# Kernel optimization log

Measured on AMD Instinct MI355X. Metric: run time of the kernel, lower is better.

Reference implementation:

```python
import jax, jax.numpy as jnp
import numpy as np

B, STREAM, IN_CH = 128, 512, 4
EXTRA, GROUPS, DEPTH = 5, 2, 3
STEP, LENGTH = 16, 32
RNN, OUT = 256, 10
C = IN_CH + 1 + EXTRA              # augmented channels: original + time + 1x1-conv
SIG_C = C + C * C + C ** 3          # signature channels per group at depth 3
W = (STREAM - LENGTH) // STEP + 1   # number of sliding windows = GRU steps
F = GROUPS * SIG_C                  # GRU input features


def _outer(a, b):
    # flattened tensor (outer) product on last axis: (...,m),(...,n)->(...,m*n)
    return (a[..., :, None] * b[..., None, :]).reshape(a.shape[:-1] + (a.shape[-1] * b.shape[-1],))


def _chen_step(S, dx):
    # Chen's identity: S <- S (tensor) exp(dx). S is a tuple of flattened
    # signature levels (..., C^k), k=1..DEPTH; dx has shape (..., C).
    P = [jnp.ones(dx.shape[:-1] + (1,), dx.dtype)]  # dx^{(x)j}/j!, j=0..DEPTH
    for j in range(1, DEPTH + 1):
        P.append(_outer(P[-1], dx) / j)
    newS = []
    for k in range(1, DEPTH + 1):
        acc = P[k]  # S_0 (x) P_k
        for j in range(k):
            acc = acc + _outer(S[k - 1 - j], P[j])
        newS.append(acc)
    return tuple(newS)


def setup_inputs() -> dict:
    key = jax.random.key(0)
    ks = jax.random.split(key, 10)
    s_aug = 1.0 / np.sqrt(IN_CH)
    s_rnn = 1.0 / np.sqrt(RNN)
    return {
        "x": jax.random.normal(ks[0], (B, STREAM, IN_CH), jnp.float32),
        "W_aug": jax.random.uniform(ks[1], (GROUPS, EXTRA, IN_CH), jnp.float32, -s_aug, s_aug),
        "b_aug": jax.random.uniform(ks[2], (GROUPS, EXTRA), jnp.float32, -s_aug, s_aug),
        "W_ih": jax.random.uniform(ks[3], (3 * RNN, F), jnp.float32, -s_rnn, s_rnn),
        "W_hh": jax.random.uniform(ks[4], (3 * RNN, RNN), jnp.float32, -s_rnn, s_rnn),
        "b_ih": jax.random.uniform(ks[5], (3 * RNN,), jnp.float32, -s_rnn, s_rnn),
        "b_hh": jax.random.uniform(ks[6], (3 * RNN,), jnp.float32, -s_rnn, s_rnn),
        "W_out": jax.random.uniform(ks[7], (OUT, RNN), jnp.float32, -s_rnn, s_rnn),
        "b_out": jax.random.uniform(ks[8], (OUT,), jnp.float32, -s_rnn, s_rnn),
    }


def reference(x, W_aug, b_aug, W_ih, W_hh, b_ih, b_hh, W_out, b_out):
    # (a) linear augmentation per channel group: [original | time | conv1x1(x)]
    t = jnp.linspace(0.0, 1.0, STREAM, dtype=x.dtype)
    t = jnp.broadcast_to(t[None, :, None], (B, STREAM, 1))
    aug = jnp.einsum('bsi,gei->bgse', x, W_aug) + b_aug[None, :, None, :]  # (B,G,S,EXTRA)
    base = jnp.broadcast_to(jnp.concatenate([x, t], -1)[:, None],
                            (B, GROUPS, STREAM, IN_CH + 1))
    xa = jnp.concatenate([base, aug], -1)            # (B,G,S,C)
    xa = xa.reshape(B * GROUPS, STREAM, C)

    # (b) depth-3 signatures over sliding windows via Chen's identity
    dx = xa[:, 1:] - xa[:, :-1]                       # (BG, S-1, C)
    widx = jnp.arange(W)[:, None] * STEP + jnp.arange(LENGTH - 1)[None, :]
    dxw = dx[:, widx]                                 # (BG, W, L-1, C)
    dxw = jnp.moveaxis(dxw, 2, 0)                     # (L-1, BG, W, C)
    S0 = tuple(jnp.zeros((B * GROUPS, W, C ** k), x.dtype) for k in range(1, DEPTH + 1))
    S, _ = jax.lax.scan(lambda S, d: (_chen_step(S, d), None), S0, dxw)
    sig = jnp.concatenate(S, -1)                      # (BG, W, SIG_C)
    sig = sig.reshape(B, GROUPS, W, SIG_C)
    sig = jnp.moveaxis(sig, 2, 0).reshape(W, B, F)    # (W, B, G*SIG_C)

    # (c) GRU over window signatures (torch.nn.GRUCell math, gate order r,z,n)
    def gru(h, xt):
        gi = xt @ W_ih.T + b_ih
        gh = h @ W_hh.T + b_hh
        ir, iz, inn = jnp.split(gi, 3, -1)
        hr, hz, hn = jnp.split(gh, 3, -1)
        r = jax.nn.sigmoid(ir + hr)
        z = jax.nn.sigmoid(iz + hz)
        n = jnp.tanh(inn + r * hn)
        return (1 - z) * n + z * h, None

    h, _ = jax.lax.scan(gru, jnp.zeros((B, RNN), x.dtype), sig)
    return jax.nn.sigmoid(h @ W_out.T + b_out)        # (B, OUT)
```

## Files before the change

kernel.cpp:

```cpp
#include <hip/hip_runtime.h>
#include <hip/hip_bf16.h>
#include <stdint.h>


typedef _Float16 f16;
typedef f16  f16x2 __attribute__((ext_vector_type(2)));
typedef f16  f16x4 __attribute__((ext_vector_type(4)));
typedef f16  f16x8 __attribute__((ext_vector_type(8)));
typedef float f32x2 __attribute__((ext_vector_type(2)));
typedef float f32x4 __attribute__((ext_vector_type(4)));

#define ASYNC16(gp, lp) __builtin_amdgcn_global_load_lds( \
    (const __attribute__((address_space(1))) void*)(gp),  \
    (__attribute__((address_space(3))) void*)(lp), 16, 0, 0)

#define BAR_LDS() do { asm volatile("s_waitcnt lgkmcnt(0)" ::: "memory"); \
                       __builtin_amdgcn_s_barrier();                      \
                       asm volatile("" ::: "memory"); } while (0)

__device__ __forceinline__ float fexp2(float x) {
    float r; asm("v_exp_f32 %0, %1" : "=v"(r) : "v"(x)); return r;
}
__device__ __forceinline__ float frcp(float x) {
    float r; asm("v_rcp_f32 %0, %1" : "=v"(r) : "v"(x)); return r;
}

__global__ __launch_bounds__(256) void prep_kernel(const float* __restrict__ x,
                                                   const float* __restrict__ W_aug,
                                                   const float* __restrict__ Wih,
                                                   const float* __restrict__ Whh,
                                                   f16* __restrict__ sig16,
                                                   f16* __restrict__ wih16,
                                                   f16* __restrict__ whh16,
                                                   uint8_t* __restrict__ whh8) {
    __shared__ float dxs[4][31][10];
    const int tid = threadIdx.x;
    if (blockIdx.x < 840) {
        int c = blockIdx.x * 256 + tid;
        int r = c / 280, kc = (c - r * 280) * 8;
        const float* src = Wih + (size_t)r * 2220 + kc;
        f16x8 o;
        if (kc + 8 <= 2220) {
            float4 v0 = *(const float4*)(src);
            float4 v1 = *(const float4*)(src + 4);
            o[0]=(f16)v0.x; o[1]=(f16)v0.y; o[2]=(f16)v0.z; o[3]=(f16)v0.w;
            o[4]=(f16)v1.x; o[5]=(f16)v1.y; o[6]=(f16)v1.z; o[7]=(f16)v1.w;
        } else {
#pragma unroll
            for (int j = 0; j < 8; j++)
                o[j] = (f16)((kc + j < 2220) ? src[j] : 0.0f);
        }
        *(f16x8*)(wih16 + (size_t)r * 2240 + kc) = o;
        return;
    }
    if (blockIdx.x < 936) {
        int c2 = ((int)blockIdx.x - 840) * 256 + tid;
        int j8 = c2 * 8;
        float w[8];
        {
            float4 v0 = *(const float4*)(Whh + j8);
            float4 v1 = *(const float4*)(Whh + j8 + 4);
            w[0]=v0.x; w[1]=v0.y; w[2]=v0.z; w[3]=v0.w;
            w[4]=v1.x; w[5]=v1.y; w[6]=v1.z; w[7]=v1.w;
        }
        f16x8 o;
#pragma unroll
        for (int j = 0; j < 8; j++) o[j] = (f16)w[j];
        *(f16x8*)(whh16 + j8) = o;
        if (j8 < 131072) {
            uint32_t p01 = (uint32_t)__builtin_amdgcn_cvt_pk_fp8_f32(w[0]*16.f, w[1]*16.f, 0, false) & 0xffffu;
            uint32_t p23 = (uint32_t)__builtin_amdgcn_cvt_pk_fp8_f32(w[2]*16.f, w[3]*16.f, 0, false) & 0xffffu;
            uint32_t p45 = (uint32_t)__builtin_amdgcn_cvt_pk_fp8_f32(w[4]*16.f, w[5]*16.f, 0, false) & 0xffffu;
            uint32_t p67 = (uint32_t)__builtin_amdgcn_cvt_pk_fp8_f32(w[6]*16.f, w[7]*16.f, 0, false) & 0xffffu;
            uint2 st = make_uint2(p01 | (p23 << 16), p45 | (p67 << 16));
            *(uint2*)(whh8 + j8) = st;
        }
        return;
    }
    const int sub = tid >> 6, t64 = tid & 63;
    const int cid = ((int)blockIdx.x - 936) * 4 + sub;
    const int w = cid % 31;
    const int bg = cid / 31;
    const int b = bg >> 1, g = bg & 1;
    if (t64 < 31) {
        int s = w * 16 + t64;
        const float4 x0 = *(const float4*)(x + ((size_t)b * 512 + s) * 4);
        const float4 x1 = *(const float4*)(x + ((size_t)b * 512 + s + 1) * 4);
        float d0 = x1.x - x0.x, d1 = x1.y - x0.y, d2 = x1.z - x0.z, d3 = x1.w - x0.w;
        dxs[sub][t64][0] = d0; dxs[sub][t64][1] = d1;
        dxs[sub][t64][2] = d2; dxs[sub][t64][3] = d3;
        dxs[sub][t64][4] = 1.0f / 511.0f;
#pragma unroll
        for (int e = 0; e < 5; e++) {
            const float* wa = W_aug + (g * 5 + e) * 4;
            dxs[sub][t64][5 + e] = d0 * wa[0] + d1 * wa[1] + d2 * wa[2] + d3 * wa[3];
        }
    }
    __syncthreads();
    size_t base = ((size_t)(w * 128 + b)) * 2240 + (size_t)g * 1110;
    if (t64 < 50) {
        int p0 = 2 * t64, p1 = p0 + 1;
        int i0 = p0 / 10, j0 = p0 % 10, j1 = j0 + 1;
        const float* dz  = &dxs[sub][0][0];
        const float* pI  = dz + i0;
        const float* pJ0 = dz + j0;
        const float* pJ1 = dz + j1;
        float s3a[10], s3b[10];
#pragma unroll
        for (int k = 0; k < 10; k++) { s3a[k] = 0.f; s3b[k] = 0.f; }
        float s2a = 0.f, s2b = 0.f, s1 = 0.f;
        for (int l = 0; l < 31; l++) {
            const float* row = dz + l * 10;
            float di  = pI[l * 10];
            float dj0 = pJ0[l * 10];
            float dj1 = pJ1[l * 10];
            float t0 = s1 + di * (1.0f / 3.0f);
            float a0 = s2a + t0 * (0.5f * dj0);
            float a1 = s2b + t0 * (0.5f * dj1);
#pragma unroll
            for (int k = 0; k < 10; k++) {
                float dk = row[k];
                s3a[k] += a0 * dk;
                s3b[k] += a1 * dk;
            }
            float u = s1 + 0.5f * di;
            s2a += u * dj0;
            s2b += u * dj1;
            s1 += di;
        }
        *(f16x2*)(sig16 + base + 10 + p0) = (f16x2){(f16)s2a, (f16)s2b};
#pragma unroll
        for (int k = 0; k < 5; k++)
            *(f16x2*)(sig16 + base + 110 + p0 * 10 + 2 * k) =
                (f16x2){(f16)s3a[2 * k], (f16)s3a[2 * k + 1]};
#pragma unroll
        for (int k = 0; k < 5; k++)
            *(f16x2*)(sig16 + base + 110 + p1 * 10 + 2 * k) =
                (f16x2){(f16)s3b[2 * k], (f16)s3b[2 * k + 1]};
    } else if (t64 < 60) {
        int c = t64 - 50;
        const float* pc = &dxs[sub][0][0] + c;
        float s = 0.f;
        for (int l = 0; l < 31; l++) s += pc[l * 10];
        sig16[base + c] = (f16)s;
    }
    if (g == 1 && t64 < 10)
        *(f16x2*)(sig16 + ((size_t)(w * 128 + b)) * 2240 + 2220 + 2 * t64) =
            (f16x2){(f16)0.0f, (f16)0.0f};
}

__global__ __launch_bounds__(512) void gemm_kernel(const f16* __restrict__ A,
                                                   const f16* __restrict__ Bw,
                                                   const float* __restrict__ bias,
                                                   const float* __restrict__ bhh,
                                                   f16* __restrict__ Cgi) {
    const int lin = blockIdx.x;
    const int t = (lin & 7) + 8 * (lin / 48);
    const int nb = (lin >> 3) % 6;
    if (t >= 31) return;
    __shared__ __align__(16) f16 As[7][128 * 32];
    __shared__ __align__(16) f16 Bs[7][128 * 32];
    const int tid = threadIdx.x, lane = tid & 63, wid = tid >> 6;
    const int wm = wid >> 2, wn = wid & 3;
    const int Mbase = t * 128, Nbase = nb * 128;
    const int lr = lane >> 2, lk = lane & 3;
    const int l16 = lane & 15, quad = lane >> 4;
    const int r0 = wid * 16;
    const f16* gaA0 = A  + (size_t)(Mbase + r0 + lr) * 2240 + lk * 8;
    const f16* gbB0 = Bw + (size_t)(Nbase + r0 + lr) * 2240 + lk * 8;

#define GISSUE(KT, BUF) do { \
        int _k0 = (KT) * 32; \
        ASYNC16(gaA0 + _k0, &As[BUF][r0 * 32]); \
        ASYNC16(gbB0 + _k0, &Bs[BUF][r0 * 32]); } while (0)

#define GCOMPUTE(BUF) do { \
        f16x8 af[4], bf[2]; \
        _Pragma("unroll") \
        for (int mt = 0; mt < 4; mt++) \
            af[mt] = *(const f16x8*)&As[BUF][(wm * 64 + mt * 16 + l16) * 32 + quad * 8]; \
        _Pragma("unroll") \
        for (int nt = 0; nt < 2; nt++) \
            bf[nt] = *(const f16x8*)&Bs[BUF][(wn * 32 + nt * 16 + l16) * 32 + quad * 8]; \
        _Pragma("unroll") \
        for (int mt = 0; mt < 4; mt++) \
            _Pragma("unroll") \
            for (int nt = 0; nt < 2; nt++) \
                acc[mt][nt] = __builtin_amdgcn_mfma_f32_16x16x32_f16(af[mt], bf[nt], acc[mt][nt], 0, 0, 0); } while (0)

    f32x4 acc[4][2];
#pragma unroll
    for (int mt = 0; mt < 4; mt++)
#pragma unroll
        for (int nt = 0; nt < 2; nt++) acc[mt][nt] = (f32x4){0.f, 0.f, 0.f, 0.f};

    GISSUE(0, 0); GISSUE(1, 1); GISSUE(2, 2);
    GISSUE(3, 3); GISSUE(4, 4); GISSUE(5, 5);
    for (int kt = 0; kt < 64; kt++) {
        asm volatile("s_waitcnt vmcnt(10) lgkmcnt(0)\n\ts_barrier" ::: "memory");
        GISSUE(kt + 6, (kt + 6) % 7);
        GCOMPUTE(kt % 7);
    }
    asm volatile("s_waitcnt vmcnt(0) lgkmcnt(0)\n\ts_barrier" ::: "memory");
    GCOMPUTE(1); GCOMPUTE(2); GCOMPUTE(3);
    GCOMPUTE(4); GCOMPUTE(5); GCOMPUTE(6);

    const float NEG_LOG2E = -1.4426950408889634f;
    const float TWO_LOG2E =  2.8853900817779268f;
#pragma unroll
    for (int mt = 0; mt < 4; mt++) {
        const int bbv = wm * 4 + mt;
#pragma unroll
        for (int nt = 0; nt < 2; nt++) {
            int col = Nbase + wn * 32 + nt * 16 + l16;
            float bvv = bias[col] + (col < 512 ? bhh[col] : 0.0f);
            float scl = (col < 512) ? NEG_LOG2E : TWO_LOG2E;
            int gs = col >> 8, hcc = col & 255;
            int gw = hcc >> 5, gtc = (hcc >> 4) & 1, gl = hcc & 15;
            int u = gs * 2 + gtc;
            int gtid = gw * 64 + quad * 16 + gl;
            size_t off = ((size_t)((t * 8 + bbv) * 6 + u)) * 2048 + (size_t)gtid * 4;
            f16x4 st;
#pragma unroll
            for (int rr = 0; rr < 4; rr++) st[rr] = (f16)((acc[mt][nt][rr] + bvv) * scl);
            *(f16x4*)(Cgi + off) = st;
        }
    }
#undef GISSUE
#undef GCOMPUTE
}

#define ACLOB \
  "a0","a1","a2","a3","a4","a5","a6","a7","a8","a9","a10","a11","a12","a13","a14","a15", \
  "a16","a17","a18","a19","a20","a21","a22","a23","a24","a25","a26","a27","a28","a29","a30","a31", \
  "a32","a33","a34","a35","a36","a37","a38","a39","a40","a41","a42","a43","a44","a45","a46","a47", \
  "a48","a49","a50","a51","a52","a53","a54","a55","a56","a57","a58","a59","a60","a61","a62","a63", \
  "a64","a65","a66","a67","a68","a69","a70","a71","a72","a73","a74","a75","a76","a77","a78","a79", \
  "a80","a81","a82","a83","a84","a85","a86","a87","a88","a89","a90","a91","a92","a93","a94","a95", \
  "a96","a97","a98","a99","a100","a101","a102","a103","a104","a105","a106","a107","a108","a109","a110","a111", \
  "a112","a113","a114","a115","a116","a117","a118","a119","a120","a121","a122","a123","a124","a125","a126","a127"

#define LF8(A0,A1, U, KT) do { \
  f32x2 _t = *(const f32x2*)(whh8 + (size_t)(((U) >> 1) * 256 + wid * 32 + ((U) & 1) * 16 + l16) * 256 + (KT) * 32 + quad * 8); \
  asm volatile("v_accvgpr_write_b32 a" #A0 ", %0\n\t" \
               "v_accvgpr_write_b32 a" #A1 ", %1" \
               :: "v"(_t[0]), "v"(_t[1]) : "a" #A0, "a" #A1); } while (0)

#define LFN(A0,A1,A2,A3, TC, KT) do { \
  f32x4 _t = *(const f32x4*)(whh16 + (size_t)(512 + wid * 32 + (TC) * 16 + l16) * 256 + (KT) * 32 + quad * 8); \
  asm volatile("v_accvgpr_write_b32 a" #A0 ", %0\n\t" \
               "v_accvgpr_write_b32 a" #A1 ", %1\n\t" \
               "v_accvgpr_write_b32 a" #A2 ", %2\n\t" \
               "v_accvgpr_write_b32 a" #A3 ", %3" \
               :: "v"(_t[0]), "v"(_t[1]), "v"(_t[2]), "v"(_t[3]) \
               : "a" #A0, "a" #A1, "a" #A2, "a" #A3); } while (0)

#define FP8GZ(P, F0,F1,F2,F3) \
  "v_mfma_f32_16x16x32_fp8_fp8 %[aR0], " P ", a[" F0 "], %[zq]\n\t" \
  "v_mfma_f32_16x16x32_fp8_fp8 %[aR1], " P ", a[" F1 "], %[zq]\n\t" \
  "v_mfma_f32_16x16x32_fp8_fp8 %[aZ0], " P ", a[" F2 "], %[zq]\n\t" \
  "v_mfma_f32_16x16x32_fp8_fp8 %[aZ1], " P ", a[" F3 "], %[zq]\n\t"

#define FP8G(P, F0,F1,F2,F3) \
  "v_mfma_f32_16x16x32_fp8_fp8 %[aR0], " P ", a[" F0 "], %[aR0]\n\t" \
  "v_mfma_f32_16x16x32_fp8_fp8 %[aR1], " P ", a[" F1 "], %[aR1]\n\t" \
  "v_mfma_f32_16x16x32_fp8_fp8 %[aZ0], " P ", a[" F2 "], %[aZ0]\n\t" \
  "v_mfma_f32_16x16x32_fp8_fp8 %[aZ1], " P ", a[" F3 "], %[aZ1]\n\t"

#define F16GZ(Q, G0,G1) \
  "v_mfma_f32_16x16x32_f16 %[aN0], " Q ", a[" G0 "], %[zq]\n\t" \
  "v_mfma_f32_16x16x32_f16 %[aN1], " Q ", a[" G1 "], %[zq]\n\t"

#define F16G(Q, G0,G1) \
  "v_mfma_f32_16x16x32_f16 %[aN0], " Q ", a[" G0 "], %[aN0]\n\t" \
  "v_mfma_f32_16x16x32_f16 %[aN1], " Q ", a[" G1 "], %[aN1]\n\t"

__global__ __launch_bounds__(512, 2) void gru_kernel(const f16* __restrict__ gi,
                                                     const f16* __restrict__ whh16,
                                                     const uint8_t* __restrict__ whh8,
                                                     const float* __restrict__ b_hh,
                                                     const float* __restrict__ W_out,
                                                     const float* __restrict__ b_out,
                                                     float* __restrict__ out) {
    __shared__ __align__(16) f16 hbufF[2][16 * 280];
    __shared__ __align__(16) uint8_t hbuf8[2][16 * 272];
    const int tid = threadIdx.x, lane = tid & 63, wid = tid >> 6;
    const int quad = lane >> 4, l16 = lane & 15;
    const int bb = blockIdx.x;

    for (int i = tid; i < 16 * 280; i += 512) hbufF[1][i] = (f16)0.0f;
    for (int i = tid; i < 16 * 272; i += 512) hbuf8[1][i] = 0;

    LF8(0,1, 0,0);   LF8(2,3, 0,1);   LF8(4,5, 0,2);   LF8(6,7, 0,3);
    LF8(8,9, 0,4);   LF8(10,11, 0,5); LF8(12,13, 0,6); LF8(14,15, 0,7);
    LF8(16,17, 1,0); LF8(18,19, 1,1); LF8(20,21, 1,2); LF8(22,23, 1,3);
    LF8(24,25, 1,4); LF8(26,27, 1,5); LF8(28,29, 1,6); LF8(30,31, 1,7);
    LF8(32,33, 2,0); LF8(34,35, 2,1); LF8(36,37, 2,2); LF8(38,39, 2,3);
    LF8(40,41, 2,4); LF8(42,43, 2,5); LF8(44,45, 2,6); LF8(46,47, 2,7);
    LF8(48,49, 3,0); LF8(50,51, 3,1); LF8(52,53, 3,2); LF8(54,55, 3,3);
    LF8(56,57, 3,4); LF8(58,59, 3,5); LF8(60,61, 3,6); LF8(62,63, 3,7);
    LFN(64,65,66,67,   0,0); LFN(68,69,70,71,   0,1); LFN(72,73,74,75,   0,2); LFN(76,77,78,79,   0,3);
    LFN(80,81,82,83,   0,4); LFN(84,85,86,87,   0,5); LFN(88,89,90,91,   0,6); LFN(92,93,94,95,   0,7);
    LFN(96,97,98,99,   1,0); LFN(100,101,102,103, 1,1); LFN(104,105,106,107, 1,2); LFN(108,109,110,111, 1,3);
    LFN(112,113,114,115, 1,4); LFN(116,117,118,119, 1,5); LFN(120,121,122,123, 1,6); LFN(124,125,126,127, 1,7);

    const float C2 = 2.8853900817779268f;
    float bhn[2];
#pragma unroll
    for (int tc = 0; tc < 2; tc++) bhn[tc] = C2 * b_hh[512 + wid * 32 + tc * 16 + l16];
    float hm[2][4];
#pragma unroll
    for (int tc = 0; tc < 2; tc++)
#pragma unroll
        for (int rr = 0; rr < 4; rr++) hm[tc][rr] = 0.f;

    uint32_t aF0 = (uint32_t)(uintptr_t)(__attribute__((address_space(3))) const void*)
                       (&hbufF[0][l16 * 280 + quad * 8]);
    uint32_t aF1 = (uint32_t)(uintptr_t)(__attribute__((address_space(3))) const void*)
                       (&hbufF[1][l16 * 280 + quad * 8]);
    uint32_t a80 = (uint32_t)(uintptr_t)(__attribute__((address_space(3))) const void*)
                       (&hbuf8[0][l16 * 272 + quad * 8]);
    uint32_t a81 = (uint32_t)(uintptr_t)(__attribute__((address_space(3))) const void*)
                       (&hbuf8[1][l16 * 272 + quad * 8]);

    const size_t lanebase = (size_t)bb * 12288 + (size_t)tid * 4;
    f16x4 gcur[6];
#pragma unroll
    for (int u = 0; u < 6; u++)
        gcur[u] = *(const f16x4*)(gi + lanebase + u * 2048);

    const f32x4 zq = (f32x4){0.f, 0.f, 0.f, 0.f};

    BAR_LDS();

    for (int t = 0; t < 31; t++) {
        const uint32_t a8 = (t & 1) ? a80 : a81;
        const uint32_t aF = (t & 1) ? aF0 : aF1;
        f32x4 aR0, aR1, aZ0, aZ1, aN0, aN1;
        f32x2 p0, p1, p2;
        f32x4 q0, q1, q2;
        asm volatile(
            "s_setprio 1\n\t"
            "ds_read_b64  %[p0], %[a8] offset:0\n\t"
            "ds_read_b128 %[q0], %[aF] offset:0\n\t"
            "ds_read_b64  %[p1], %[a8] offset:32\n\t"
            "ds_read_b128 %[q1], %[aF] offset:64\n\t"
            "ds_read_b64  %[p2], %[a8] offset:64\n\t"
            "ds_read_b128 %[q2], %[aF] offset:128\n\t"
            "s_waitcnt lgkmcnt(5)\n\t"
            FP8GZ("%[p0]", "0:1","16:17","32:33","48:49")
            "ds_read_b64  %[p0], %[a8] offset:96\n\t"
            "s_waitcnt lgkmcnt(5)\n\t"
            F16GZ("%[q0]", "64:67","96:99")
            "ds_read_b128 %[q0], %[aF] offset:192\n\t"
            "s_waitcnt lgkmcnt(5)\n\t"
            FP8G("%[p1]", "2:3","18:19","34:35","50:51")
            "ds_read_b64  %[p1], %[a8] offset:128\n\t"
            "s_waitcnt lgkmcnt(5)\n\t"
            F16G("%[q1]", "68:71","100:103")
            "ds_read_b128 %[q1], %[aF] offset:256\n\t"
            "s_waitcnt lgkmcnt(5)\n\t"
            FP8G("%[p2]", "4:5","20:21","36:37","52:53")
            "ds_read_b64  %[p2], %[a8] offset:160\n\t"
            "s_waitcnt lgkmcnt(5)\n\t"
            F16G("%[q2]", "72:75","104:107")
            "ds_read_b128 %[q2], %[aF] offset:320\n\t"
            "s_waitcnt lgkmcnt(5)\n\t"
            FP8G("%[p0]", "6:7","22:23","38:39","54:55")
            "ds_read_b64  %[p0], %[a8] offset:192\n\t"
            "s_waitcnt lgkmcnt(5)\n\t"
            F16G("%[q0]", "76:79","108:111")
            "ds_read_b128 %[q0], %[aF] offset:384\n\t"
            "s_waitcnt lgkmcnt(5)\n\t"
            FP8G("%[p1]", "8:9","24:25","40:41","56:57")
            "ds_read_b64  %[p1], %[a8] offset:224\n\t"
            "s_waitcnt lgkmcnt(5)\n\t"
            F16G("%[q1]", "80:83","112:115")
            "ds_read_b128 %[q1], %[aF] offset:448\n\t"
            "s_waitcnt lgkmcnt(5)\n\t"
            FP8G("%[p2]", "10:11","26:27","42:43","58:59")
            "s_waitcnt lgkmcnt(4)\n\t"
            F16G("%[q2]", "84:87","116:119")
            "s_waitcnt lgkmcnt(3)\n\t"
            FP8G("%[p0]", "12:13","28:29","44:45","60:61")
            "s_waitcnt lgkmcnt(2)\n\t"
            F16G("%[q0]", "88:91","120:123")
            "s_waitcnt lgkmcnt(1)\n\t"
            FP8G("%[p1]", "14:15","30:31","46:47","62:63")
            "s_waitcnt lgkmcnt(0)\n\t"
            F16G("%[q1]", "92:95","124:127")
            "s_setprio 0\n\t"
            "s_nop 7\n\ts_nop 7"
            : [aR0]"=&v"(aR0), [aR1]"=&v"(aR1), [aZ0]"=&v"(aZ0), [aZ1]"=&v"(aZ1),
              [aN0]"=&v"(aN0), [aN1]"=&v"(aN1),
              [p0]"=&v"(p0), [p1]"=&v"(p1), [p2]"=&v"(p2),
              [q0]"=&v"(q0), [q1]"=&v"(q1), [q2]"=&v"(q2)
            : [a8]"v"(a8), [aF]"v"(aF), [zq]"v"(zq)
            : ACLOB);

        f16* hdF = hbufF[t & 1];
        uint8_t* hd8 = hbuf8[t & 1];
        const float C1N16 = -0.09016844005556021f;
#pragma unroll
        for (int tc = 0; tc < 2; tc++) {
            const int hcx = wid * 32 + tc * 16 + l16;
            const f32x4 vR = tc ? aR1 : aR0;
            const f32x4 vZ = tc ? aZ1 : aZ0;
            const f32x4 vN = tc ? aN1 : aN0;
#pragma unroll
            for (int rr = 0; rr < 4; rr++) {
                float rg = frcp(1.f + fexp2(fmaf(C1N16, vR[rr], (float)gcur[tc][rr])));
                float zg = frcp(1.f + fexp2(fmaf(C1N16, vZ[rr], (float)gcur[2 + tc][rr])));
                float t2 = fmaf(rg, fmaf(C2, vN[rr], bhn[tc]), (float)gcur[4 + tc][rr]);
                float e2 = fexp2(t2);
                float ng = fmaf(-2.f, frcp(e2 + 1.f), 1.f);
                float h  = fmaf(zg, hm[tc][rr] - ng, ng);
                hm[tc][rr] = h;
                hdF[(quad * 4 + rr) * 280 + hcx] = (f16)h;
                int pk = __builtin_amdgcn_cvt_pk_fp8_f32(h, h, 0, false);
                hd8[(quad * 4 + rr) * 272 + hcx] = (uint8_t)pk;
            }
        }
        {
            int tn = (t < 30) ? t + 1 : 30;
            const f16* gsrc = gi + (size_t)tn * 98304 + lanebase;
#pragma unroll
            for (int u = 0; u < 6; u++)
                gcur[u] = *(const f16x4*)(gsrc + u * 2048);
        }
        BAR_LDS();
    }
    if (tid < 160) {
        int r = tid / 10, oc = tid - r * 10;
        const f16* hfin = hbufF[0];
        float s = b_out[oc];
        for (int k = 0; k < 256; k++) s += (float)hfin[r * 280 + k] * W_out[oc * 256 + k];
        out[(bb * 16 + r) * 10 + oc] = frcp(1.f + __expf(-s));
    }
}

extern "C" void kernel_launch(void* const* d_in, const int* in_sizes, int n_in,
                              void* d_out, int out_size, void* d_ws, size_t ws_size,
                              hipStream_t stream) {
    const float* x     = (const float*)d_in[0];
    const float* W_aug = (const float*)d_in[1];
    const float* W_ih  = (const float*)d_in[3];
    const float* W_hh  = (const float*)d_in[4];
    const float* b_ih  = (const float*)d_in[5];
    const float* b_hh  = (const float*)d_in[6];
    const float* W_out = (const float*)d_in[7];
    const float* b_out = (const float*)d_in[8];
    float* out = (float*)d_out;

    char* ws = (char*)d_ws;
    const size_t SIG_BYTES  = (size_t)3968 * 2240 * 2;
    const size_t WIH_BYTES  = (size_t)768 * 2240 * 2;
    const size_t WHH_BYTES  = (size_t)768 * 256 * 2;
    const size_t WHH8_BYTES = (size_t)512 * 256;
    const size_t GI_BYTES   = (size_t)31 * 8 * 6 * 512 * 4 * 2;
    if (ws_size < SIG_BYTES + WIH_BYTES + WHH_BYTES + WHH8_BYTES + GI_BYTES) return;
    f16* sig16    = (f16*)ws;
    f16* wih16    = (f16*)(ws + SIG_BYTES);
    f16* whh16    = (f16*)(ws + SIG_BYTES + WIH_BYTES);
    uint8_t* whh8 = (uint8_t*)(ws + SIG_BYTES + WIH_BYTES + WHH_BYTES);
    f16* giw      = (f16*)(ws + SIG_BYTES + WIH_BYTES + WHH_BYTES + WHH8_BYTES);

    hipLaunchKernelGGL(prep_kernel, dim3(2920), dim3(256), 0, stream,
                       x, W_aug, W_ih, W_hh, sig16, wih16, whh16, whh8);
    hipLaunchKernelGGL(gemm_kernel, dim3(192), dim3(512), 0, stream,
                       sig16, wih16, b_ih, b_hh, giw);
    hipLaunchKernelGGL(gru_kernel, dim3(8), dim3(512), 0, stream,
                       giw, whh16, whh8, b_hh, W_out, b_out, out);
}
```

Baseline: 200.0 us.

## Fuse input GEMM and GRU kernels with an atomic completion counter

```diff
diff --git a/kernel.cpp b/kernel.cpp
--- a/kernel.cpp
+++ b/kernel.cpp
@@ -32,7 +32,8 @@
                                                    f16* __restrict__ sig16,
                                                    f16* __restrict__ wih16,
                                                    f16* __restrict__ whh16,
-                                                   uint8_t* __restrict__ whh8) {
+                                                   uint8_t* __restrict__ whh8,
+                                                   unsigned int* __restrict__ done) {
     __shared__ float dxs[4][31][10];
     const int tid = threadIdx.x;
     if (blockIdx.x < 840) {
@@ -54,6 +55,7 @@
         return;
     }
     if (blockIdx.x < 936) {
+        if (blockIdx.x == 840 && tid == 0) *done = 0u;
         int c2 = ((int)blockIdx.x - 840) * 256 + tid;
         int j8 = c2 * 8;
         float w[8];
@@ -149,25 +151,80 @@
             (f16x2){(f16)0.0f, (f16)0.0f};
 }
 
-__global__ __launch_bounds__(512) void gemm_kernel(const f16* __restrict__ A,
-                                                   const f16* __restrict__ Bw,
-                                                   const float* __restrict__ bias,
-                                                   const float* __restrict__ bhh,
-                                                   f16* __restrict__ Cgi) {
-    const int lin = blockIdx.x;
-    const int t = (lin & 7) + 8 * (lin / 48);
-    const int nb = (lin >> 3) % 6;
-    if (t >= 31) return;
+#define ACLOB \
+  "a0","a1","a2","a3","a4","a5","a6","a7","a8","a9","a10","a11","a12","a13","a14","a15", \
+  "a16","a17","a18","a19","a20","a21","a22","a23","a24","a25","a26","a27","a28","a29","a30","a31", \
+  "a32","a33","a34","a35","a36","a37","a38","a39","a40","a41","a42","a43","a44","a45","a46","a47", \
+  "a48","a49","a50","a51","a52","a53","a54","a55","a56","a57","a58","a59","a60","a61","a62","a63", \
+  "a64","a65","a66","a67","a68","a69","a70","a71","a72","a73","a74","a75","a76","a77","a78","a79", \
+  "a80","a81","a82","a83","a84","a85","a86","a87","a88","a89","a90","a91","a92","a93","a94","a95", \
+  "a96","a97","a98","a99","a100","a101","a102","a103","a104","a105","a106","a107","a108","a109","a110","a111", \
+  "a112","a113","a114","a115","a116","a117","a118","a119","a120","a121","a122","a123","a124","a125","a126","a127"
+
+#define LF8(A0,A1, U, KT) do { \
+  f32x2 _t = *(const f32x2*)(whh8 + (size_t)(((U) >> 1) * 256 + wid * 32 + ((U) & 1) * 16 + l16) * 256 + (KT) * 32 + quad * 8); \
+  asm volatile("v_accvgpr_write_b32 a" #A0 ", %0\n\t" \
+               "v_accvgpr_write_b32 a" #A1 ", %1" \
+               :: "v"(_t[0]), "v"(_t[1]) : "a" #A0, "a" #A1); } while (0)
+
+#define LFN(A0,A1,A2,A3, TC, KT) do { \
+  f32x4 _t = *(const f32x4*)(whh16 + (size_t)(512 + wid * 32 + (TC) * 16 + l16) * 256 + (KT) * 32 + quad * 8); \
+  asm volatile("v_accvgpr_write_b32 a" #A0 ", %0\n\t" \
+               "v_accvgpr_write_b32 a" #A1 ", %1\n\t" \
+               "v_accvgpr_write_b32 a" #A2 ", %2\n\t" \
+               "v_accvgpr_write_b32 a" #A3 ", %3" \
+               :: "v"(_t[0]), "v"(_t[1]), "v"(_t[2]), "v"(_t[3]) \
+               : "a" #A0, "a" #A1, "a" #A2, "a" #A3); } while (0)
+
+#define FP8GZ(P, F0,F1,F2,F3) \
+  "v_mfma_f32_16x16x32_fp8_fp8 %[aR0], " P ", a[" F0 "], %[zq]\n\t" \
+  "v_mfma_f32_16x16x32_fp8_fp8 %[aR1], " P ", a[" F1 "], %[zq]\n\t" \
+  "v_mfma_f32_16x16x32_fp8_fp8 %[aZ0], " P ", a[" F2 "], %[zq]\n\t" \
+  "v_mfma_f32_16x16x32_fp8_fp8 %[aZ1], " P ", a[" F3 "], %[zq]\n\t"
+
+#define FP8G(P, F0,F1,F2,F3) \
+  "v_mfma_f32_16x16x32_fp8_fp8 %[aR0], " P ", a[" F0 "], %[aR0]\n\t" \
+  "v_mfma_f32_16x16x32_fp8_fp8 %[aR1], " P ", a[" F1 "], %[aR1]\n\t" \
+  "v_mfma_f32_16x16x32_fp8_fp8 %[aZ0], " P ", a[" F2 "], %[aZ0]\n\t" \
+  "v_mfma_f32_16x16x32_fp8_fp8 %[aZ1], " P ", a[" F3 "], %[aZ1]\n\t"
+
+#define F16GZ(Q, G0,G1) \
+  "v_mfma_f32_16x16x32_f16 %[aN0], " Q ", a[" G0 "], %[zq]\n\t" \
+  "v_mfma_f32_16x16x32_f16 %[aN1], " Q ", a[" G1 "], %[zq]\n\t"
+
+#define F16G(Q, G0,G1) \
+  "v_mfma_f32_16x16x32_f16 %[aN0], " Q ", a[" G0 "], %[aN0]\n\t" \
+  "v_mfma_f32_16x16x32_f16 %[aN1], " Q ", a[" G1 "], %[aN1]\n\t"
+
+__global__ __launch_bounds__(512, 2) void fused_kernel(const f16* __restrict__ A,
+                                                       const f16* __restrict__ Bw,
+                                                       const float* __restrict__ bias,
+                                                       const float* __restrict__ bhh,
+                                                       f16* __restrict__ Cgi,
+                                                       const f16* __restrict__ whh16,
+                                                       const uint8_t* __restrict__ whh8,
+                                                       const float* __restrict__ W_out,
+                                                       const float* __restrict__ b_out,
+                                                       float* __restrict__ out,
+                                                       unsigned int* __restrict__ done) {
     __shared__ __align__(16) f16 As[7][128 * 32];
     __shared__ __align__(16) f16 Bs[7][128 * 32];
+    __shared__ __align__(16) f16 hbufF[2][16 * 280];
+    __shared__ __align__(16) uint8_t hbuf8[2][16 * 272];
     const int tid = threadIdx.x, lane = tid & 63, wid = tid >> 6;
-    const int wm = wid >> 2, wn = wid & 3;
-    const int Mbase = t * 128, Nbase = nb * 128;
-    const int lr = lane >> 2, lk = lane & 3;
-    const int l16 = lane & 15, quad = lane >> 4;
-    const int r0 = wid * 16;
-    const f16* gaA0 = A  + (size_t)(Mbase + r0 + lr) * 2240 + lk * 8;
-    const f16* gbB0 = Bw + (size_t)(Nbase + r0 + lr) * 2240 + lk * 8;
+    const int quad = lane >> 4, l16 = lane & 15;
+
+    if (blockIdx.x < 192) {
+        const int lin = blockIdx.x;
+        const int t = (lin & 7) + 8 * (lin / 48);
+        const int nb = (lin >> 3) % 6;
+        if (t >= 31) return;
+        const int wm = wid >> 2, wn = wid & 3;
+        const int Mbase = t * 128, Nbase = nb * 128;
+        const int lr = lane >> 2, lk = lane & 3;
+        const int r0 = wid * 16;
+        const f16* gaA0 = A  + (size_t)(Mbase + r0 + lr) * 2240 + lk * 8;
+        const f16* gbB0 = Bw + (size_t)(Nbase + r0 + lr) * 2240 + lk * 8;
 
 #define GISSUE(KT, BUF) do { \
         int _k0 = (KT) * 32; \
@@ -188,105 +245,54 @@
             for (int nt = 0; nt < 2; nt++) \
                 acc[mt][nt] = __builtin_amdgcn_mfma_f32_16x16x32_f16(af[mt], bf[nt], acc[mt][nt], 0, 0, 0); } while (0)
 
-    f32x4 acc[4][2];
-#pragma unroll
-    for (int mt = 0; mt < 4; mt++)
-#pragma unroll
-        for (int nt = 0; nt < 2; nt++) acc[mt][nt] = (f32x4){0.f, 0.f, 0.f, 0.f};
-
-    GISSUE(0, 0); GISSUE(1, 1); GISSUE(2, 2);
-    GISSUE(3, 3); GISSUE(4, 4); GISSUE(5, 5);
-    for (int kt = 0; kt < 64; kt++) {
-        asm volatile("s_waitcnt vmcnt(10) lgkmcnt(0)\n\ts_barrier" ::: "memory");
-        GISSUE(kt + 6, (kt + 6) % 7);
-        GCOMPUTE(kt % 7);
-    }
-    asm volatile("s_waitcnt vmcnt(0) lgkmcnt(0)\n\ts_barrier" ::: "memory");
-    GCOMPUTE(1); GCOMPUTE(2); GCOMPUTE(3);
-    GCOMPUTE(4); GCOMPUTE(5); GCOMPUTE(6);
-
-    const float NEG_LOG2E = -1.4426950408889634f;
-    const float TWO_LOG2E =  2.8853900817779268f;
-#pragma unroll
-    for (int mt = 0; mt < 4; mt++) {
-        const int bbv = wm * 4 + mt;
-#pragma unroll
-        for (int nt = 0; nt < 2; nt++) {
-            int col = Nbase + wn * 32 + nt * 16 + l16;
-            float bvv = bias[col] + (col < 512 ? bhh[col] : 0.0f);
-            float scl = (col < 512) ? NEG_LOG2E : TWO_LOG2E;
-            int gs = col >> 8, hcc = col & 255;
-            int gw = hcc >> 5, gtc = (hcc >> 4) & 1, gl = hcc & 15;
-            int u = gs * 2 + gtc;
-            int gtid = gw * 64 + quad * 16 + gl;
-            size_t off = ((size_t)((t * 8 + bbv) * 6 + u)) * 2048 + (size_t)gtid * 4;
-            f16x4 st;
-#pragma unroll
-            for (int rr = 0; rr < 4; rr++) st[rr] = (f16)((acc[mt][nt][rr] + bvv) * scl);
-            *(f16x4*)(Cgi + off) = st;
-        }
-    }
+        f32x4 acc[4][2];
+#pragma unroll
+        for (int mt = 0; mt < 4; mt++)
+#pragma unroll
+            for (int nt = 0; nt < 2; nt++) acc[mt][nt] = (f32x4){0.f, 0.f, 0.f, 0.f};
+
+        GISSUE(0, 0); GISSUE(1, 1); GISSUE(2, 2);
+        GISSUE(3, 3); GISSUE(4, 4); GISSUE(5, 5);
+        for (int kt = 0; kt < 64; kt++) {
+            asm volatile("s_waitcnt vmcnt(10) lgkmcnt(0)\n\ts_barrier" ::: "memory");
+            GISSUE(kt + 6, (kt + 6) % 7);
+            GCOMPUTE(kt % 7);
+        }
+        asm volatile("s_waitcnt vmcnt(0) lgkmcnt(0)\n\ts_barrier" ::: "memory");
+        GCOMPUTE(1); GCOMPUTE(2); GCOMPUTE(3);
+        GCOMPUTE(4); GCOMPUTE(5); GCOMPUTE(6);
+
+        const float NEG_LOG2E = -1.4426950408889634f;
+        const float TWO_LOG2E =  2.8853900817779268f;
+#pragma unroll
+        for (int mt = 0; mt < 4; mt++) {
+            const int bbv = wm * 4 + mt;
+#pragma unroll
+            for (int nt = 0; nt < 2; nt++) {
+                int col = Nbase + wn * 32 + nt * 16 + l16;
+                float bvv = bias[col] + (col < 512 ? bhh[col] : 0.0f);
+                float scl = (col < 512) ? NEG_LOG2E : TWO_LOG2E;
+                int gs = col >> 8, hcc = col & 255;
+                int gw = hcc >> 5, gtc = (hcc >> 4) & 1, gl = hcc & 15;
+                int u = gs * 2 + gtc;
+                int gtid = gw * 64 + quad * 16 + gl;
+                size_t off = ((size_t)((t * 8 + bbv) * 6 + u)) * 2048 + (size_t)gtid * 4;
+                f16x4 st;
+#pragma unroll
+                for (int rr = 0; rr < 4; rr++) st[rr] = (f16)((acc[mt][nt][rr] + bvv) * scl);
+                *(f16x4*)(Cgi + off) = st;
+            }
+        }
+        __threadfence();
+        __syncthreads();
+        if (tid == 0) atomicAdd(done, 1u);
+        return;
 #undef GISSUE
 #undef GCOMPUTE
-}
-
-#define ACLOB \
-  "a0","a1","a2","a3","a4","a5","a6","a7","a8","a9","a10","a11","a12","a13","a14","a15", \
-  "a16","a17","a18","a19","a20","a21","a22","a23","a24","a25","a26","a27","a28","a29","a30","a31", \
-  "a32","a33","a34","a35","a36","a37","a38","a39","a40","a41","a42","a43","a44","a45","a46","a47", \
-  "a48","a49","a50","a51","a52","a53","a54","a55","a56","a57","a58","a59","a60","a61","a62","a63", \
-  "a64","a65","a66","a67","a68","a69","a70","a71","a72","a73","a74","a75","a76","a77","a78","a79", \
-  "a80","a81","a82","a83","a84","a85","a86","a87","a88","a89","a90","a91","a92","a93","a94","a95", \
-  "a96","a97","a98","a99","a100","a101","a102","a103","a104","a105","a106","a107","a108","a109","a110","a111", \
-  "a112","a113","a114","a115","a116","a117","a118","a119","a120","a121","a122","a123","a124","a125","a126","a127"
-
-#define LF8(A0,A1, U, KT) do { \
-  f32x2 _t = *(const f32x2*)(whh8 + (size_t)(((U) >> 1) * 256 + wid * 32 + ((U) & 1) * 16 + l16) * 256 + (KT) * 32 + quad * 8); \
-  asm volatile("v_accvgpr_write_b32 a" #A0 ", %0\n\t" \
-               "v_accvgpr_write_b32 a" #A1 ", %1" \
-               :: "v"(_t[0]), "v"(_t[1]) : "a" #A0, "a" #A1); } while (0)
-
-#define LFN(A0,A1,A2,A3, TC, KT) do { \
-  f32x4 _t = *(const f32x4*)(whh16 + (size_t)(512 + wid * 32 + (TC) * 16 + l16) * 256 + (KT) * 32 + quad * 8); \
-  asm volatile("v_accvgpr_write_b32 a" #A0 ", %0\n\t" \
-               "v_accvgpr_write_b32 a" #A1 ", %1\n\t" \
-               "v_accvgpr_write_b32 a" #A2 ", %2\n\t" \
-               "v_accvgpr_write_b32 a" #A3 ", %3" \
-               :: "v"(_t[0]), "v"(_t[1]), "v"(_t[2]), "v"(_t[3]) \
-               : "a" #A0, "a" #A1, "a" #A2, "a" #A3); } while (0)
-
-#define FP8GZ(P, F0,F1,F2,F3) \
-  "v_mfma_f32_16x16x32_fp8_fp8 %[aR0], " P ", a[" F0 "], %[zq]\n\t" \
-  "v_mfma_f32_16x16x32_fp8_fp8 %[aR1], " P ", a[" F1 "], %[zq]\n\t" \
-  "v_mfma_f32_16x16x32_fp8_fp8 %[aZ0], " P ", a[" F2 "], %[zq]\n\t" \
-  "v_mfma_f32_16x16x32_fp8_fp8 %[aZ1], " P ", a[" F3 "], %[zq]\n\t"
-
-#define FP8G(P, F0,F1,F2,F3) \
-  "v_mfma_f32_16x16x32_fp8_fp8 %[aR0], " P ", a[" F0 "], %[aR0]\n\t" \
-  "v_mfma_f32_16x16x32_fp8_fp8 %[aR1], " P ", a[" F1 "], %[aR1]\n\t" \
-  "v_mfma_f32_16x16x32_fp8_fp8 %[aZ0], " P ", a[" F2 "], %[aZ0]\n\t" \
-  "v_mfma_f32_16x16x32_fp8_fp8 %[aZ1], " P ", a[" F3 "], %[aZ1]\n\t"
-
-#define F16GZ(Q, G0,G1) \
-  "v_mfma_f32_16x16x32_f16 %[aN0], " Q ", a[" G0 "], %[zq]\n\t" \
-  "v_mfma_f32_16x16x32_f16 %[aN1], " Q ", a[" G1 "], %[zq]\n\t"
-
-#define F16G(Q, G0,G1) \
-  "v_mfma_f32_16x16x32_f16 %[aN0], " Q ", a[" G0 "], %[aN0]\n\t" \
-  "v_mfma_f32_16x16x32_f16 %[aN1], " Q ", a[" G1 "], %[aN1]\n\t"
-
-__global__ __launch_bounds__(512, 2) void gru_kernel(const f16* __restrict__ gi,
-                                                     const f16* __restrict__ whh16,
-                                                     const uint8_t* __restrict__ whh8,
-                                                     const float* __restrict__ b_hh,
-                                                     const float* __restrict__ W_out,
-                                                     const float* __restrict__ b_out,
-                                                     float* __restrict__ out) {
-    __shared__ __align__(16) f16 hbufF[2][16 * 280];
-    __shared__ __align__(16) uint8_t hbuf8[2][16 * 272];
-    const int tid = threadIdx.x, lane = tid & 63, wid = tid >> 6;
-    const int quad = lane >> 4, l16 = lane & 15;
-    const int bb = blockIdx.x;
+    }
+
+    const int bb = (int)blockIdx.x - 192;
+    const f16* gi = Cgi;
 
     for (int i = tid; i < 16 * 280; i += 512) hbufF[1][i] = (f16)0.0f;
     for (int i = tid; i < 16 * 272; i += 512) hbuf8[1][i] = 0;
@@ -307,7 +313,7 @@
     const float C2 = 2.8853900817779268f;
     float bhn[2];
 #pragma unroll
-    for (int tc = 0; tc < 2; tc++) bhn[tc] = C2 * b_hh[512 + wid * 32 + tc * 16 + l16];
+    for (int tc = 0; tc < 2; tc++) bhn[tc] = C2 * bhh[512 + wid * 32 + tc * 16 + l16];
     float hm[2][4];
 #pragma unroll
     for (int tc = 0; tc < 2; tc++)
@@ -322,6 +328,12 @@
                        (&hbuf8[0][l16 * 272 + quad * 8]);
     uint32_t a81 = (uint32_t)(uintptr_t)(__attribute__((address_space(3))) const void*)
                        (&hbuf8[1][l16 * 272 + quad * 8]);
+
+    if (tid == 0) {
+        while (atomicAdd(done, 0u) < 186u) __builtin_amdgcn_s_sleep(8);
+    }
+    __syncthreads();
+    __threadfence();
 
     const size_t lanebase = (size_t)bb * 12288 + (size_t)tid * 4;
     f16x4 gcur[6];
@@ -458,17 +470,17 @@
     const size_t WHH_BYTES  = (size_t)768 * 256 * 2;
     const size_t WHH8_BYTES = (size_t)512 * 256;
     const size_t GI_BYTES   = (size_t)31 * 8 * 6 * 512 * 4 * 2;
-    if (ws_size < SIG_BYTES + WIH_BYTES + WHH_BYTES + WHH8_BYTES + GI_BYTES) return;
+    const size_t DONE_BYTES = 64;
+    if (ws_size < SIG_BYTES + WIH_BYTES + WHH_BYTES + WHH8_BYTES + GI_BYTES + DONE_BYTES) return;
     f16* sig16    = (f16*)ws;
     f16* wih16    = (f16*)(ws + SIG_BYTES);
     f16* whh16    = (f16*)(ws + SIG_BYTES + WIH_BYTES);
     uint8_t* whh8 = (uint8_t*)(ws + SIG_BYTES + WIH_BYTES + WHH_BYTES);
     f16* giw      = (f16*)(ws + SIG_BYTES + WIH_BYTES + WHH_BYTES + WHH8_BYTES);
+    unsigned int* done = (unsigned int*)(ws + SIG_BYTES + WIH_BYTES + WHH_BYTES + WHH8_BYTES + GI_BYTES);
 
     hipLaunchKernelGGL(prep_kernel, dim3(2920), dim3(256), 0, stream,
-                       x, W_aug, W_ih, W_hh, sig16, wih16, whh16, whh8);
-    hipLaunchKernelGGL(gemm_kernel, dim3(192), dim3(512), 0, stream,
-                       sig16, wih16, b_ih, b_hh, giw);
-    hipLaunchKernelGGL(gru_kernel, dim3(8), dim3(512), 0, stream,
-                       giw, whh16, whh8, b_hh, W_out, b_out, out);
+                       x, W_aug, W_ih, W_hh, sig16, wih16, whh16, whh8, done);
+    hipLaunchKernelGGL(fused_kernel, dim3(200), dim3(512), 0, stream,
+                       sig16, wih16, b_ih, b_hh, giw, whh16, whh8, W_out, b_out, out, done);
 }
```

Measured after the change: 220.1 us. 1.1x slower.

## Stage signature rows in LDS for coalesced stores; retile input GEMM to 64-row blocks

Applied to the files above, without the earlier changes.

```diff
diff --git a/kernel.cpp b/kernel.cpp
--- a/kernel.cpp
+++ b/kernel.cpp
@@ -34,6 +34,7 @@
                                                    f16* __restrict__ whh16,
                                                    uint8_t* __restrict__ whh8) {
     __shared__ float dxs[4][31][10];
+    __shared__ f16 srow[4][1112];
     const int tid = threadIdx.x;
     if (blockIdx.x < 840) {
         int c = blockIdx.x * 256 + tid;
@@ -128,60 +129,63 @@
             s2b += u * dj1;
             s1 += di;
         }
-        *(f16x2*)(sig16 + base + 10 + p0) = (f16x2){(f16)s2a, (f16)s2b};
+        *(f16x2*)&srow[sub][10 + p0] = (f16x2){(f16)s2a, (f16)s2b};
 #pragma unroll
         for (int k = 0; k < 5; k++)
-            *(f16x2*)(sig16 + base + 110 + p0 * 10 + 2 * k) =
+            *(f16x2*)&srow[sub][110 + p0 * 10 + 2 * k] =
                 (f16x2){(f16)s3a[2 * k], (f16)s3a[2 * k + 1]};
 #pragma unroll
         for (int k = 0; k < 5; k++)
-            *(f16x2*)(sig16 + base + 110 + p1 * 10 + 2 * k) =
+            *(f16x2*)&srow[sub][110 + p1 * 10 + 2 * k] =
                 (f16x2){(f16)s3b[2 * k], (f16)s3b[2 * k + 1]};
     } else if (t64 < 60) {
         int c = t64 - 50;
         const float* pc = &dxs[sub][0][0] + c;
         float s = 0.f;
         for (int l = 0; l < 31; l++) s += pc[l * 10];
-        sig16[base + c] = (f16)s;
-    }
+        srow[sub][c] = (f16)s;
+    }
+    __syncthreads();
+    for (int j = t64; j < 555; j += 64)
+        *(f16x2*)(sig16 + base + 2 * j) = *(const f16x2*)&srow[sub][2 * j];
     if (g == 1 && t64 < 10)
         *(f16x2*)(sig16 + ((size_t)(w * 128 + b)) * 2240 + 2220 + 2 * t64) =
             (f16x2){(f16)0.0f, (f16)0.0f};
 }
 
-__global__ __launch_bounds__(512) void gemm_kernel(const f16* __restrict__ A,
+__global__ __launch_bounds__(256) void gemm_kernel(const f16* __restrict__ A,
                                                    const f16* __restrict__ Bw,
                                                    const float* __restrict__ bias,
                                                    const float* __restrict__ bhh,
                                                    f16* __restrict__ Cgi) {
     const int lin = blockIdx.x;
-    const int t = (lin & 7) + 8 * (lin / 48);
-    const int nb = (lin >> 3) % 6;
-    if (t >= 31) return;
-    __shared__ __align__(16) f16 As[7][128 * 32];
-    __shared__ __align__(16) f16 Bs[7][128 * 32];
+    const int nb = lin % 6;
+    const int mb = lin / 6;
+    const int t = mb >> 1, half = mb & 1;
+    __shared__ __align__(16) f16 As[6][64 * 32];
+    __shared__ __align__(16) f16 Bs[6][128 * 32];
     const int tid = threadIdx.x, lane = tid & 63, wid = tid >> 6;
-    const int wm = wid >> 2, wn = wid & 3;
-    const int Mbase = t * 128, Nbase = nb * 128;
-    const int lr = lane >> 2, lk = lane & 3;
     const int l16 = lane & 15, quad = lane >> 4;
-    const int r0 = wid * 16;
-    const f16* gaA0 = A  + (size_t)(Mbase + r0 + lr) * 2240 + lk * 8;
-    const f16* gbB0 = Bw + (size_t)(Nbase + r0 + lr) * 2240 + lk * 8;
+    const int lrow = lane >> 2, lk = lane & 3;
+    const int Nbase = nb * 128;
+    const f16* gaA  = A  + (size_t)(t * 128 + half * 64 + wid * 16 + lrow) * 2240 + lk * 8;
+    const f16* gbB0 = Bw + (size_t)(Nbase + wid * 32 + lrow) * 2240 + lk * 8;
+    const f16* gbB1 = Bw + (size_t)(Nbase + wid * 32 + 16 + lrow) * 2240 + lk * 8;
 
 #define GISSUE(KT, BUF) do { \
         int _k0 = (KT) * 32; \
-        ASYNC16(gaA0 + _k0, &As[BUF][r0 * 32]); \
-        ASYNC16(gbB0 + _k0, &Bs[BUF][r0 * 32]); } while (0)
+        ASYNC16(gaA  + _k0, &As[BUF][(wid * 16) * 32]); \
+        ASYNC16(gbB0 + _k0, &Bs[BUF][(wid * 32) * 32]); \
+        ASYNC16(gbB1 + _k0, &Bs[BUF][(wid * 32 + 16) * 32]); } while (0)
 
 #define GCOMPUTE(BUF) do { \
         f16x8 af[4], bf[2]; \
         _Pragma("unroll") \
         for (int mt = 0; mt < 4; mt++) \
-            af[mt] = *(const f16x8*)&As[BUF][(wm * 64 + mt * 16 + l16) * 32 + quad * 8]; \
+            af[mt] = *(const f16x8*)&As[BUF][(mt * 16 + l16) * 32 + quad * 8]; \
         _Pragma("unroll") \
         for (int nt = 0; nt < 2; nt++) \
-            bf[nt] = *(const f16x8*)&Bs[BUF][(wn * 32 + nt * 16 + l16) * 32 + quad * 8]; \
+            bf[nt] = *(const f16x8*)&Bs[BUF][(wid * 32 + nt * 16 + l16) * 32 + quad * 8]; \
         _Pragma("unroll") \
         for (int mt = 0; mt < 4; mt++) \
             _Pragma("unroll") \
@@ -194,25 +198,23 @@
 #pragma unroll
         for (int nt = 0; nt < 2; nt++) acc[mt][nt] = (f32x4){0.f, 0.f, 0.f, 0.f};
 
-    GISSUE(0, 0); GISSUE(1, 1); GISSUE(2, 2);
-    GISSUE(3, 3); GISSUE(4, 4); GISSUE(5, 5);
-    for (int kt = 0; kt < 64; kt++) {
-        asm volatile("s_waitcnt vmcnt(10) lgkmcnt(0)\n\ts_barrier" ::: "memory");
-        GISSUE(kt + 6, (kt + 6) % 7);
-        GCOMPUTE(kt % 7);
+    GISSUE(0, 0); GISSUE(1, 1); GISSUE(2, 2); GISSUE(3, 3); GISSUE(4, 4);
+    for (int kt = 0; kt < 65; kt++) {
+        asm volatile("s_waitcnt vmcnt(12) lgkmcnt(0)\n\ts_barrier" ::: "memory");
+        GISSUE(kt + 5, (kt + 5) % 6);
+        GCOMPUTE(kt % 6);
     }
     asm volatile("s_waitcnt vmcnt(0) lgkmcnt(0)\n\ts_barrier" ::: "memory");
-    GCOMPUTE(1); GCOMPUTE(2); GCOMPUTE(3);
-    GCOMPUTE(4); GCOMPUTE(5); GCOMPUTE(6);
+    GCOMPUTE(5); GCOMPUTE(0); GCOMPUTE(1); GCOMPUTE(2); GCOMPUTE(3);
 
     const float NEG_LOG2E = -1.4426950408889634f;
     const float TWO_LOG2E =  2.8853900817779268f;
 #pragma unroll
     for (int mt = 0; mt < 4; mt++) {
-        const int bbv = wm * 4 + mt;
+        const int bbv = half * 4 + mt;
 #pragma unroll
         for (int nt = 0; nt < 2; nt++) {
-            int col = Nbase + wn * 32 + nt * 16 + l16;
+            int col = Nbase + wid * 32 + nt * 16 + l16;
             float bvv = bias[col] + (col < 512 ? bhh[col] : 0.0f);
             float scl = (col < 512) ? NEG_LOG2E : TWO_LOG2E;
             int gs = col >> 8, hcc = col & 255;
@@ -467,7 +469,7 @@
 
     hipLaunchKernelGGL(prep_kernel, dim3(2920), dim3(256), 0, stream,
                        x, W_aug, W_ih, W_hh, sig16, wih16, whh16, whh8);
-    hipLaunchKernelGGL(gemm_kernel, dim3(192), dim3(512), 0, stream,
+    hipLaunchKernelGGL(gemm_kernel, dim3(372), dim3(256), 0, stream,
                        sig16, wih16, b_ih, b_hh, giw);
     hipLaunchKernelGGL(gru_kernel, dim3(8), dim3(512), 0, stream,
                        giw, whh16, whh8, b_hh, W_out, b_out, out);
```

New measurement: 200.1 us. Within noise of the previous version (+0.1%).
